# Performance work log

Hardware: AMD Instinct MI355X
Metric: run time of the kernel (lower is better)

Reference implementation:

```python
import jax, jax.numpy as jnp
import numpy as np

N = 50000      # nodes
E = 800000     # edges
IN = 128       # in_channels
H = 64         # hidden (= edge_dim)
OUT = 64       # out_channels
BN_EPS = 1e-5


def _bn(h, gamma, beta):
    # BatchNorm1d in training mode: per-feature batch statistics
    mu = h.mean(axis=0)
    var = h.var(axis=0)
    return gamma * (h - mu) * jax.lax.rsqrt(var + BN_EPS) + beta


def _gine_layer(x, src, dst, edge_attr, We, be, W1, b1, g, bb, W2, b2):
    # edge_attr projected to node feature dim: [E, d_in]
    ea = edge_attr @ We.T + be
    # message: relu(x_j + lin(edge_attr)); x_j = x[src]
    m = jax.nn.relu(x[src] + ea)
    # scatter-add aggregate at destination nodes
    agg = jax.ops.segment_sum(m, dst, num_segments=x.shape[0])
    # (1 + eps) * x_r with eps = 0
    out = agg + x
    # MLP: Linear -> BN -> ReLU -> Linear
    h = jax.nn.relu(_bn(out @ W1.T + b1, g, bb))
    return h @ W2.T + b2


def setup_inputs() -> dict:
    key = jax.random.key(0)
    ks = jax.random.split(key, 12)

    def glorot(k, shape):
        return jax.random.normal(k, shape, jnp.float32) / np.float32(np.sqrt(shape[1]))

    return {
        "x": jax.random.normal(ks[0], (N, IN), jnp.float32),
        "edge_index": jax.random.randint(ks[1], (2, E), 0, N, jnp.int64),
        "edge_attr": jax.random.normal(ks[2], (E, H), jnp.float32),
        # layer 0
        "We0": glorot(ks[3], (IN, H)), "be0": jnp.zeros((IN,), jnp.float32),
        "W1_0": glorot(ks[4], (H, IN)), "b1_0": jnp.zeros((H,), jnp.float32),
        "g0": jnp.ones((H,), jnp.float32), "bb0": jnp.zeros((H,), jnp.float32),
        "W2_0": glorot(ks[5], (H, H)), "b2_0": jnp.zeros((H,), jnp.float32),
        # layer 1
        "We1": glorot(ks[6], (H, H)), "be1": jnp.zeros((H,), jnp.float32),
        "W1_1": glorot(ks[7], (H, H)), "b1_1": jnp.zeros((H,), jnp.float32),
        "g1": jnp.ones((H,), jnp.float32), "bb1": jnp.zeros((H,), jnp.float32),
        "W2_1": glorot(ks[8], (OUT, H)), "b2_1": jnp.zeros((OUT,), jnp.float32),
    }


def reference(x, edge_index, edge_attr,
              We0, be0, W1_0, b1_0, g0, bb0, W2_0, b2_0,
              We1, be1, W1_1, b1_1, g1, bb1, W2_1, b2_1):
    src, dst = edge_index[0], edge_index[1]
    h = _gine_layer(x, src, dst, edge_attr, We0, be0, W1_0, b1_0, g0, bb0, W2_0, b2_0)
    h = jax.nn.relu(h)  # dropout p=0.0 -> identity
    return _gine_layer(h, src, dst, edge_attr, We1, be1, W1_1, b1_1, g1, bb1, W2_1, b2_1)
```

## Files before the change

kernel.cpp:

```cpp
#include <hip/hip_runtime.h>
#include <hip/hip_bf16.h>


typedef short bhalf4 __attribute__((ext_vector_type(4)));
typedef short short8 __attribute__((ext_vector_type(8)));
typedef float f32x4 __attribute__((ext_vector_type(4)));
typedef float f32x2 __attribute__((ext_vector_type(2)));

__device__ __forceinline__ short f2bf(float x) {
    unsigned u = __float_as_uint(x);
    unsigned r = (u + 0x7fffu + ((u >> 16) & 1u)) >> 16;
    return (short)r;
}
__device__ __forceinline__ float bf2f(unsigned short u) {
    return __uint_as_float(((unsigned)u) << 16);
}

__global__ __launch_bounds__(256) void hist_kernel(
    const int* __restrict__ ei, int* __restrict__ cnt, int E)
{
    int e = blockIdx.x * 256 + threadIdx.x;
    if (e < E) atomicAdd(&cnt[ei[E + e]], 1);
}

__global__ __launch_bounds__(1024) void scan_kernel(
    const int* __restrict__ cnt, int* __restrict__ offs,
    int* __restrict__ cursor, int N)
{
    __shared__ int wsum[16];
    __shared__ int chunk_base;
    int tid = threadIdx.x;
    int lane = tid & 63, wid = tid >> 6;
    if (tid == 0) chunk_base = 0;
    __syncthreads();
    for (int start = 0; start < N; start += 1024) {
        int i = start + tid;
        int v = (i < N) ? cnt[i] : 0;
        int s = v;
#pragma unroll
        for (int d = 1; d < 64; d <<= 1) {
            int t = __shfl_up(s, d);
            if (lane >= d) s += t;
        }
        if (lane == 63) wsum[wid] = s;
        __syncthreads();
        int wbase = 0;
        for (int w = 0; w < wid; ++w) wbase += wsum[w];
        int excl = chunk_base + wbase + s - v;
        if (i < N) { offs[i] = excl; cursor[i] = excl; }
        int tot = 0;
        for (int w = 0; w < 16; ++w) tot += wsum[w];
        __syncthreads();
        if (tid == 0) chunk_base += tot;
        __syncthreads();
    }
    if (threadIdx.x == 0) offs[N] = chunk_base;
}

__global__ __launch_bounds__(256) void scatter_kernel(
    const int* __restrict__ ei, int* __restrict__ cursor,
    int* __restrict__ inv, int E)
{
    int e = blockIdx.x * 256 + threadIdx.x;
    if (e >= E) return;
    int d = ei[E + e];
    int pos = atomicAdd(&cursor[d], 1);
    inv[e] = pos;
}

__global__ __launch_bounds__(256) void xcast_kernel(
    const float* __restrict__ x, unsigned short* __restrict__ xb, int total)
{
    for (int i = blockIdx.x * 256 + threadIdx.x; i < total; i += gridDim.x * 256)
        xb[i] = (unsigned short)f2bf(x[i]);
}

template<int DF>
__global__ __launch_bounds__(256) void edgem_kernel(
    const unsigned short* __restrict__ xb,
    const int*    __restrict__ ei,
    const float*  __restrict__ eattr,
    const short*  __restrict__ WB,
    const float*  __restrict__ be,
    const int*    __restrict__ inv,
    unsigned short* __restrict__ pbuf,
    int E)
{
    constexpr int FC  = DF / 16;
    constexpr int LPR = DF / 8;
    constexpr int RPI = 64 / LPR;
    constexpr int NI  = 16 / RPI;
    __shared__ short cm[4][16][DF];
    const int wave = threadIdx.x >> 6;
    const int lane = threadIdx.x & 63;
    const int ebase = (blockIdx.x * 4 + wave) * 16;
    if (ebase >= E) return;
    const int g = lane >> 4, c = lane & 15;
    short* ct = &cm[wave][0][0];
    auto sw = [](int s, int r) { return s ^ ((r >> 1) & 7); };

    int spos[NI], rr[NI], qq[NI];
    short8 xrv[NI];
#pragma unroll
    for (int i = 0; i < NI; ++i) {
        int r = i * RPI + lane / LPR;
        int q = lane % LPR;
        rr[i] = r; qq[i] = q;
        int e = ebase + r;
        bool v = e < E;
        int es = v ? e : (E - 1);
        spos[i] = v ? inv[es] : -1;
        int se = ei[es];
        xrv[i] = *(const short8*)(xb + (size_t)se * DF + q * 8);
    }

    {
        int r = lane >> 2, q = lane & 3;
        int e = ebase + r;
        const float* src = eattr + (size_t)((e < E) ? e : (E - 1)) * 64;
#pragma unroll
        for (int i = 0; i < 4; ++i) {
            f32x4 v = *(const f32x4*)(src + i * 16 + q * 4);
            bhalf4 b;
            b[0] = f2bf(v[0]); b[1] = f2bf(v[1]); b[2] = f2bf(v[2]); b[3] = f2bf(v[3]);
            int s = i * 2 + (q >> 1), h = q & 1;
            *(bhalf4*)(ct + r * DF + sw(s, r) * 8 + h * 4) = b;
        }
    }
    asm volatile("s_waitcnt lgkmcnt(0)" ::: "memory");
    __builtin_amdgcn_sched_barrier(0);

    short8 bfr0 = *(const short8*)(ct + c * DF + sw(g, c) * 8);
    short8 bfr1 = *(const short8*)(ct + c * DF + sw(g + 4, c) * 8);

    f32x4 acc[FC];
#pragma unroll
    for (int fc = 0; fc < FC; ++fc) {
        const short* aw = WB + (size_t)(fc * 16 + c) * 64 + g * 8;
        short8 aw0 = *(const short8*)(aw);
        short8 aw1 = *(const short8*)(aw + 32);
        f32x4 a = {0.f, 0.f, 0.f, 0.f};
        a = __builtin_amdgcn_mfma_f32_16x16x32_bf16(aw0, bfr0, a, 0, 0, 0);
        a = __builtin_amdgcn_mfma_f32_16x16x32_bf16(aw1, bfr1, a, 0, 0, 0);
        acc[fc] = a;
    }

#pragma unroll
    for (int fc = 0; fc < FC; ++fc) {
        f32x4 bev = *(const f32x4*)(be + fc * 16 + g * 4);
        bhalf4 mo;
#pragma unroll
        for (int r = 0; r < 4; ++r)
            mo[r] = f2bf(acc[fc][r] + bev[r]);
        int s = fc * 2 + (g >> 1), h = g & 1;
        *(bhalf4*)(ct + c * DF + sw(s, c) * 8 + h * 4) = mo;
    }
    asm volatile("s_waitcnt lgkmcnt(0)" ::: "memory");
    __builtin_amdgcn_sched_barrier(0);

#pragma unroll
    for (int i = 0; i < NI; ++i) {
        int r = rr[i], q = qq[i];
        short8 v = *(const short8*)(ct + r * DF + sw(q, r) * 8);
        short8 o;
#pragma unroll
        for (int j = 0; j < 8; ++j) {
            float f = bf2f((unsigned short)v[j]) + bf2f((unsigned short)xrv[i][j]);
            o[j] = f2bf(fmaxf(f, 0.f));
        }
        if (spos[i] >= 0)
            *(short8*)(pbuf + (size_t)spos[i] * DF + q * 8) = o;
    }
}

__global__ __launch_bounds__(256) void gathersum0_kernel(
    const unsigned short* __restrict__ pbuf,
    const int* __restrict__ offs,
    const float* __restrict__ x,
    unsigned short* __restrict__ sb, int N)
{
    int wid = threadIdx.x >> 6, lane = threadIdx.x & 63;
    int n = blockIdx.x * 4 + wid;
    if (n >= N) return;
    f32x2 xx = *(const f32x2*)(x + (size_t)n * 128 + 2 * lane);
    float s0 = xx[0], s1 = xx[1];
    int i0 = offs[n], i1 = offs[n + 1];
    const unsigned int* p = (const unsigned int*)(pbuf + (size_t)i0 * 128) + lane;
    int cnt = i1 - i0;
    int i = 0;
    for (; i + 3 < cnt; i += 4) {
        unsigned int v0 = p[0], v1 = p[64], v2 = p[128], v3 = p[192];
        s0 += bf2f((unsigned short)v0) + bf2f((unsigned short)v1)
            + bf2f((unsigned short)v2) + bf2f((unsigned short)v3);
        s1 += bf2f((unsigned short)(v0 >> 16)) + bf2f((unsigned short)(v1 >> 16))
            + bf2f((unsigned short)(v2 >> 16)) + bf2f((unsigned short)(v3 >> 16));
        p += 256;
    }
    for (; i < cnt; ++i) {
        unsigned int v = p[0];
        s0 += bf2f((unsigned short)v);
        s1 += bf2f((unsigned short)(v >> 16));
        p += 64;
    }
    unsigned int packed = (unsigned int)(unsigned short)f2bf(s0)
                        | ((unsigned int)(unsigned short)f2bf(s1) << 16);
    *(unsigned int*)(sb + (size_t)n * 128 + 2 * lane) = packed;
}

__global__ __launch_bounds__(256) void gathersum1_kernel(
    const unsigned short* __restrict__ pbuf,
    const int* __restrict__ offs,
    const float* __restrict__ y0, unsigned short* __restrict__ sb, int N)
{
    int wid = threadIdx.x >> 6, lane = threadIdx.x & 63;
    int n = blockIdx.x * 4 + wid;
    if (n >= N) return;
    float s = y0[(size_t)n * 64 + lane];
    int i0 = offs[n], i1 = offs[n + 1];
    const unsigned short* p = pbuf + (size_t)i0 * 64 + lane;
    int cnt = i1 - i0;
    int i = 0;
    for (; i + 3 < cnt; i += 4) {
        s += bf2f(p[0]) + bf2f(p[64]) + bf2f(p[128]) + bf2f(p[192]);
        p += 256;
    }
    for (; i < cnt; ++i) { s += bf2f(p[0]); p += 64; }
    sb[(size_t)n * 64 + lane] = (unsigned short)f2bf(s);
}

template<int DIN>
__global__ __launch_bounds__(256) void ngemm_kernel(
    const unsigned short* __restrict__ A,
    const short* __restrict__ W, const float* __restrict__ b,
    float* __restrict__ out, int N)
{
    constexpr int KK = DIN / 32;
    const int wave = threadIdx.x >> 6;
    const int lane = threadIdx.x & 63;
    const int nbase = (blockIdx.x * 4 + wave) * 16;
    if (nbase >= N) return;
    const int g = lane >> 4, c = lane & 15;

    int rowc = nbase + c; if (rowc >= N) rowc = N - 1;
    const unsigned short* arow = A + (size_t)rowc * DIN + g * 8;
    short8 afr[KK];
#pragma unroll
    for (int kk = 0; kk < KK; ++kk)
        afr[kk] = *(const short8*)(arow + kk * 32);

#pragma unroll
    for (int cc = 0; cc < 4; ++cc) {
        const float bev = b[cc * 16 + c];
        f32x4 acc = {bev, bev, bev, bev};
#pragma unroll
        for (int kk = 0; kk < KK; ++kk) {
            short8 bw = *(const short8*)(W + (size_t)(cc * 16 + c) * DIN + kk * 32 + g * 8);
            acc = __builtin_amdgcn_mfma_f32_16x16x32_bf16(afr[kk], bw, acc, 0, 0, 0);
        }
#pragma unroll
        for (int r = 0; r < 4; ++r) {
            int row = nbase + g * 4 + r;
            if (row < N) out[(size_t)row * 64 + cc * 16 + c] = acc[r];
        }
    }
}

__global__ __launch_bounds__(256) void ngemm_bn_kernel(
    const float* __restrict__ t, const float* __restrict__ scsh,
    const short* __restrict__ W2, const float* __restrict__ b2,
    float* __restrict__ out, unsigned short* __restrict__ outb,
    int N, int relu_out)
{
    const int wave = threadIdx.x >> 6;
    const int lane = threadIdx.x & 63;
    const int nbase = (blockIdx.x * 4 + wave) * 16;
    if (nbase >= N) return;
    const int g = lane >> 4, c = lane & 15;

    int rowc = nbase + c; if (rowc >= N) rowc = N - 1;
    const float* trow = t + (size_t)rowc * 64 + g * 8;

    short8 afr[2];
#pragma unroll
    for (int kk = 0; kk < 2; ++kk) {
        f32x4 q0 = *(const f32x4*)(trow + kk * 32);
        f32x4 q1 = *(const f32x4*)(trow + kk * 32 + 4);
        const int kbase = kk * 32 + g * 8;
        f32x4 sc0 = *(const f32x4*)(scsh + kbase);
        f32x4 sc1 = *(const f32x4*)(scsh + kbase + 4);
        f32x4 sh0 = *(const f32x4*)(scsh + 64 + kbase);
        f32x4 sh1 = *(const f32x4*)(scsh + 64 + kbase + 4);
#pragma unroll
        for (int j = 0; j < 4; ++j) {
            afr[kk][j]     = f2bf(fmaxf(q0[j] * sc0[j] + sh0[j], 0.f));
            afr[kk][j + 4] = f2bf(fmaxf(q1[j] * sc1[j] + sh1[j], 0.f));
        }
    }

#pragma unroll
    for (int cc = 0; cc < 4; ++cc) {
        const float bev = b2[cc * 16 + c];
        f32x4 acc = {bev, bev, bev, bev};
#pragma unroll
        for (int kk = 0; kk < 2; ++kk) {
            short8 bw = *(const short8*)(W2 + (size_t)(cc * 16 + c) * 64 + kk * 32 + g * 8);
            acc = __builtin_amdgcn_mfma_f32_16x16x32_bf16(afr[kk], bw, acc, 0, 0, 0);
        }
#pragma unroll
        for (int r = 0; r < 4; ++r) {
            int row = nbase + g * 4 + r;
            if (row < N) {
                float v = acc[r];
                if (relu_out) {
                    v = fmaxf(v, 0.f);
                    outb[(size_t)row * 64 + cc * 16 + c] = (unsigned short)f2bf(v);
                }
                out[(size_t)row * 64 + cc * 16 + c] = v;
            }
        }
    }
}

__global__ __launch_bounds__(256) void bnstats_kernel(
    const float* __restrict__ t, float* __restrict__ sums, int total)
{
    int tid = threadIdx.x;
    float s = 0.f, s2 = 0.f;
    for (int i = blockIdx.x * 256 + tid; i < total; i += gridDim.x * 256) {
        float v = t[i];
        s += v; s2 += v * v;
    }
    __shared__ float ls[256], ls2[256];
    ls[tid] = s; ls2[tid] = s2;
    __syncthreads();
    if (tid < 64) {
        s  = ls[tid]  + ls[tid + 64]  + ls[tid + 128]  + ls[tid + 192];
        s2 = ls2[tid] + ls2[tid + 64] + ls2[tid + 128] + ls2[tid + 192];
        atomicAdd(&sums[tid], s);
        atomicAdd(&sums[64 + tid], s2);
    }
}

__global__ void bnfinal_kernel(const float* __restrict__ sums,
                               const float* __restrict__ g,
                               const float* __restrict__ bb,
                               float* __restrict__ scsh, float invN)
{
    int f = threadIdx.x;
    float mean = sums[f] * invN;
    float var  = sums[64 + f] * invN - mean * mean;
    float sc = g[f] * rsqrtf(var + 1e-5f);
    scsh[f] = sc;
    scsh[64 + f] = bb[f] - mean * sc;
}

__global__ __launch_bounds__(256) void prep_kernel(
    const float* __restrict__ We0, const float* __restrict__ W1_0,
    const float* __restrict__ We1, const float* __restrict__ W1_1,
    const float* __restrict__ W2_0, const float* __restrict__ W2_1,
    short* __restrict__ WeB0, short* __restrict__ W1B0,
    short* __restrict__ WeB1, short* __restrict__ W1B1,
    short* __restrict__ W2B0, short* __restrict__ W2B1)
{
    int i = blockIdx.x * 256 + threadIdx.x;
    if (i < 128 * 64) WeB0[i] = f2bf(We0[i]);
    if (i < 64 * 128) W1B0[i] = f2bf(W1_0[i]);
    if (i < 64 * 64) {
        WeB1[i] = f2bf(We1[i]);
        W1B1[i] = f2bf(W1_1[i]);
        W2B0[i] = f2bf(W2_0[i]);
        W2B1[i] = f2bf(W2_1[i]);
    }
}

extern "C" void kernel_launch(void* const* d_in, const int* in_sizes, int n_in,
                              void* d_out, int out_size, void* d_ws, size_t ws_size,
                              hipStream_t stream)
{
    (void)n_in; (void)out_size; (void)ws_size;
    const float* x     = (const float*)d_in[0];
    const int*   ei    = (const int*)d_in[1];
    const float* eattr = (const float*)d_in[2];
    const float* We0   = (const float*)d_in[3];
    const float* be0   = (const float*)d_in[4];
    const float* W1_0  = (const float*)d_in[5];
    const float* b1_0  = (const float*)d_in[6];
    const float* g0    = (const float*)d_in[7];
    const float* bb0   = (const float*)d_in[8];
    const float* W2_0  = (const float*)d_in[9];
    const float* b2_0  = (const float*)d_in[10];
    const float* We1   = (const float*)d_in[11];
    const float* be1   = (const float*)d_in[12];
    const float* W1_1  = (const float*)d_in[13];
    const float* b1_1  = (const float*)d_in[14];
    const float* g1    = (const float*)d_in[15];
    const float* bb1   = (const float*)d_in[16];
    const float* W2_1  = (const float*)d_in[17];
    const float* b2_1  = (const float*)d_in[18];
    float* out = (float*)d_out;

    const int N = in_sizes[0] / 128;
    const int E = in_sizes[2] / 64;

    char* ws = (char*)d_ws;
    size_t o = 0;
    auto alloc = [&](size_t bytes) { char* p = ws + o; o = (o + bytes + 255) & ~(size_t)255; return p; };
    unsigned short* pbuf = (unsigned short*)alloc((size_t)E * 128 * 2);
    float* tbuf   = (float*)alloc((size_t)N * 64 * 4);
    float* y0     = (float*)alloc((size_t)N * 64 * 4);
    unsigned short* xb = (unsigned short*)alloc((size_t)N * 128 * 2);
    unsigned short* yb = (unsigned short*)alloc((size_t)N * 64 * 2);
    short* WeB0   = (short*)alloc(128 * 64 * 2);
    short* W1B0   = (short*)alloc(64 * 128 * 2);
    short* WeB1   = (short*)alloc(64 * 64 * 2);
    short* W1B1   = (short*)alloc(64 * 64 * 2);
    short* W2B0   = (short*)alloc(64 * 64 * 2);
    short* W2B1   = (short*)alloc(64 * 64 * 2);
    float* stats  = (float*)alloc(512 * 4);
    int*   cnt    = (int*)alloc((size_t)N * 4);
    int*   offs   = (int*)alloc((size_t)(N + 1) * 4);
    int*   inv    = (int*)alloc((size_t)E * 4);
    float* sum0  = stats;
    float* scsh0 = stats + 128;
    float* sum1  = stats + 256;
    float* scsh1 = stats + 384;
    unsigned short* sb0 = xb;
    unsigned short* sb1 = yb;

    (void)hipMemsetAsync(stats, 0, 512 * 4, stream);
    (void)hipMemsetAsync(cnt, 0, (size_t)N * 4, stream);
    prep_kernel<<<64, 256, 0, stream>>>(We0, W1_0, We1, W1_1, W2_0, W2_1,
                                        WeB0, W1B0, WeB1, W1B1, W2B0, W2B1);
    xcast_kernel<<<2048, 256, 0, stream>>>(x, xb, N * 128);

    const int eb256 = (E + 255) / 256;

    hist_kernel<<<eb256, 256, 0, stream>>>(ei, cnt, E);
    scan_kernel<<<1, 1024, 0, stream>>>(cnt, offs, cnt, N);
    scatter_kernel<<<eb256, 256, 0, stream>>>(ei, cnt, inv, E);

    const int edge_blocks = ((E + 15) / 16 + 3) / 4;
    const int n4_blocks   = (N + 3) / 4;
    const int nt_blocks   = ((N + 15) / 16 + 3) / 4;

    edgem_kernel<128><<<edge_blocks, 256, 0, stream>>>(
        xb, ei, eattr, WeB0, be0, inv, pbuf, E);
    gathersum0_kernel<<<n4_blocks, 256, 0, stream>>>(pbuf, offs, x, sb0, N);
    ngemm_kernel<128><<<nt_blocks, 256, 0, stream>>>(sb0, W1B0, b1_0, tbuf, N);
    bnstats_kernel<<<256, 256, 0, stream>>>(tbuf, sum0, N * 64);
    bnfinal_kernel<<<1, 64, 0, stream>>>(sum0, g0, bb0, scsh0, 1.0f / N);
    ngemm_bn_kernel<<<nt_blocks, 256, 0, stream>>>(
        tbuf, scsh0, W2B0, b2_0, y0, yb, N, 1);

    edgem_kernel<64><<<edge_blocks, 256, 0, stream>>>(
        yb, ei, eattr, WeB1, be1, inv, pbuf, E);
    gathersum1_kernel<<<n4_blocks, 256, 0, stream>>>(pbuf, offs, y0, sb1, N);
    ngemm_kernel<64><<<nt_blocks, 256, 0, stream>>>(sb1, W1B1, b1_1, tbuf, N);
    bnstats_kernel<<<256, 256, 0, stream>>>(tbuf, sum1, N * 64);
    bnfinal_kernel<<<1, 64, 0, stream>>>(sum1, g1, bb1, scsh1, 1.0f / N);
    ngemm_bn_kernel<<<nt_blocks, 256, 0, stream>>>(
        tbuf, scsh1, W2B1, b2_1, out, yb, N, 0);
}
```

Before: 534.5 us.

## Fuse BN statistics into GEMM epilogue and merge prep/cast kernels

The node GEMM now accumulates per-feature sum and sum-of-squares in its epilogue using shuffles and atomics, which removes the separate bnstats pass over tbuf. The BN scale/shift is recomputed inside the second GEMM, which removes the bnfinal launch. Weight conversion and the x cast are merged into one launch. The edge kernel now issues the eattr load and LDS staging before the gathers and uses a changed swizzle. In exchange there are many more global atomics on 128 addresses and redundant per-thread rsqrt work.

```diff
diff --git a/kernel.cpp b/kernel.cpp
--- a/kernel.cpp
+++ b/kernel.cpp
@@ -68,11 +68,26 @@
     inv[e] = pos;
 }
 
-__global__ __launch_bounds__(256) void xcast_kernel(
+__global__ __launch_bounds__(256) void prep_kernel(
+    const float* __restrict__ We0, const float* __restrict__ W1_0,
+    const float* __restrict__ We1, const float* __restrict__ W1_1,
+    const float* __restrict__ W2_0, const float* __restrict__ W2_1,
+    short* __restrict__ WeB0, short* __restrict__ W1B0,
+    short* __restrict__ WeB1, short* __restrict__ W1B1,
+    short* __restrict__ W2B0, short* __restrict__ W2B1,
     const float* __restrict__ x, unsigned short* __restrict__ xb, int total)
 {
-    for (int i = blockIdx.x * 256 + threadIdx.x; i < total; i += gridDim.x * 256)
-        xb[i] = (unsigned short)f2bf(x[i]);
+    int i = blockIdx.x * 256 + threadIdx.x;
+    if (i < 128 * 64) WeB0[i] = f2bf(We0[i]);
+    if (i < 64 * 128) W1B0[i] = f2bf(W1_0[i]);
+    if (i < 64 * 64) {
+        WeB1[i] = f2bf(We1[i]);
+        W1B1[i] = f2bf(W1_1[i]);
+        W2B0[i] = f2bf(W2_0[i]);
+        W2B1[i] = f2bf(W2_1[i]);
+    }
+    for (int k = i; k < total; k += gridDim.x * 256)
+        xb[k] = (unsigned short)f2bf(x[k]);
 }
 
 template<int DF>
@@ -97,7 +112,21 @@
     if (ebase >= E) return;
     const int g = lane >> 4, c = lane & 15;
     short* ct = &cm[wave][0][0];
-    auto sw = [](int s, int r) { return s ^ ((r >> 1) & 7); };
+    auto sw = [](int s, int r) { return s ^ (r & 7); };
+
+    {
+        int r = lane >> 2, q = lane & 3;
+        int e = ebase + r;
+        const float* src = eattr + (size_t)((e < E) ? e : (E - 1)) * 64;
+#pragma unroll
+        for (int i = 0; i < 4; ++i) {
+            f32x4 v = *(const f32x4*)(src + i * 16 + q * 4);
+            bhalf4 b;
+            b[0] = f2bf(v[0]); b[1] = f2bf(v[1]); b[2] = f2bf(v[2]); b[3] = f2bf(v[3]);
+            int s = i * 2 + (q >> 1), h = q & 1;
+            *(bhalf4*)(ct + r * DF + sw(s, r) * 8 + h * 4) = b;
+        }
+    }
 
     int spos[NI], rr[NI], qq[NI];
     short8 xrv[NI];
@@ -112,20 +141,6 @@
         spos[i] = v ? inv[es] : -1;
         int se = ei[es];
         xrv[i] = *(const short8*)(xb + (size_t)se * DF + q * 8);
-    }
-
-    {
-        int r = lane >> 2, q = lane & 3;
-        int e = ebase + r;
-        const float* src = eattr + (size_t)((e < E) ? e : (E - 1)) * 64;
-#pragma unroll
-        for (int i = 0; i < 4; ++i) {
-            f32x4 v = *(const f32x4*)(src + i * 16 + q * 4);
-            bhalf4 b;
-            b[0] = f2bf(v[0]); b[1] = f2bf(v[1]); b[2] = f2bf(v[2]); b[3] = f2bf(v[3]);
-            int s = i * 2 + (q >> 1), h = q & 1;
-            *(bhalf4*)(ct + r * DF + sw(s, r) * 8 + h * 4) = b;
-        }
     }
     asm volatile("s_waitcnt lgkmcnt(0)" ::: "memory");
     __builtin_amdgcn_sched_barrier(0);
@@ -232,7 +247,7 @@
 __global__ __launch_bounds__(256) void ngemm_kernel(
     const unsigned short* __restrict__ A,
     const short* __restrict__ W, const float* __restrict__ b,
-    float* __restrict__ out, int N)
+    float* __restrict__ out, float* __restrict__ sums, int N)
 {
     constexpr int KK = DIN / 32;
     const int wave = threadIdx.x >> 6;
@@ -257,19 +272,31 @@
             short8 bw = *(const short8*)(W + (size_t)(cc * 16 + c) * DIN + kk * 32 + g * 8);
             acc = __builtin_amdgcn_mfma_f32_16x16x32_bf16(afr[kk], bw, acc, 0, 0, 0);
         }
+        float sv = 0.f, qv = 0.f;
 #pragma unroll
         for (int r = 0; r < 4; ++r) {
             int row = nbase + g * 4 + r;
-            if (row < N) out[(size_t)row * 64 + cc * 16 + c] = acc[r];
+            if (row < N) {
+                float v = acc[r];
+                out[(size_t)row * 64 + cc * 16 + c] = v;
+                sv += v; qv += v * v;
+            }
+        }
+        sv += __shfl_xor(sv, 16); sv += __shfl_xor(sv, 32);
+        qv += __shfl_xor(qv, 16); qv += __shfl_xor(qv, 32);
+        if (g == 0) {
+            atomicAdd(&sums[cc * 16 + c], sv);
+            atomicAdd(&sums[64 + cc * 16 + c], qv);
         }
     }
 }
 
 __global__ __launch_bounds__(256) void ngemm_bn_kernel(
-    const float* __restrict__ t, const float* __restrict__ scsh,
+    const float* __restrict__ t, const float* __restrict__ sums,
+    const float* __restrict__ gam, const float* __restrict__ bet,
     const short* __restrict__ W2, const float* __restrict__ b2,
     float* __restrict__ out, unsigned short* __restrict__ outb,
-    int N, int relu_out)
+    int N, int relu_out, float invN)
 {
     const int wave = threadIdx.x >> 6;
     const int lane = threadIdx.x & 63;
@@ -286,14 +313,15 @@
         f32x4 q0 = *(const f32x4*)(trow + kk * 32);
         f32x4 q1 = *(const f32x4*)(trow + kk * 32 + 4);
         const int kbase = kk * 32 + g * 8;
-        f32x4 sc0 = *(const f32x4*)(scsh + kbase);
-        f32x4 sc1 = *(const f32x4*)(scsh + kbase + 4);
-        f32x4 sh0 = *(const f32x4*)(scsh + 64 + kbase);
-        f32x4 sh1 = *(const f32x4*)(scsh + 64 + kbase + 4);
-#pragma unroll
-        for (int j = 0; j < 4; ++j) {
-            afr[kk][j]     = f2bf(fmaxf(q0[j] * sc0[j] + sh0[j], 0.f));
-            afr[kk][j + 4] = f2bf(fmaxf(q1[j] * sc1[j] + sh1[j], 0.f));
+#pragma unroll
+        for (int j = 0; j < 8; ++j) {
+            int f = kbase + j;
+            float mean = sums[f] * invN;
+            float var  = sums[64 + f] * invN - mean * mean;
+            float sc = gam[f] * rsqrtf(var + 1e-5f);
+            float sh = bet[f] - mean * sc;
+            float q = (j < 4) ? q0[j] : q1[j - 4];
+            afr[kk][j] = f2bf(fmaxf(q * sc + sh, 0.f));
         }
     }
 
@@ -318,58 +346,6 @@
                 out[(size_t)row * 64 + cc * 16 + c] = v;
             }
         }
-    }
-}
-
-__global__ __launch_bounds__(256) void bnstats_kernel(
-    const float* __restrict__ t, float* __restrict__ sums, int total)
-{
-    int tid = threadIdx.x;
-    float s = 0.f, s2 = 0.f;
-    for (int i = blockIdx.x * 256 + tid; i < total; i += gridDim.x * 256) {
-        float v = t[i];
-        s += v; s2 += v * v;
-    }
-    __shared__ float ls[256], ls2[256];
-    ls[tid] = s; ls2[tid] = s2;
-    __syncthreads();
-    if (tid < 64) {
-        s  = ls[tid]  + ls[tid + 64]  + ls[tid + 128]  + ls[tid + 192];
-        s2 = ls2[tid] + ls2[tid + 64] + ls2[tid + 128] + ls2[tid + 192];
-        atomicAdd(&sums[tid], s);
-        atomicAdd(&sums[64 + tid], s2);
-    }
-}
-
-__global__ void bnfinal_kernel(const float* __restrict__ sums,
-                               const float* __restrict__ g,
-                               const float* __restrict__ bb,
-                               float* __restrict__ scsh, float invN)
-{
-    int f = threadIdx.x;
-    float mean = sums[f] * invN;
-    float var  = sums[64 + f] * invN - mean * mean;
-    float sc = g[f] * rsqrtf(var + 1e-5f);
-    scsh[f] = sc;
-    scsh[64 + f] = bb[f] - mean * sc;
-}
-
-__global__ __launch_bounds__(256) void prep_kernel(
-    const float* __restrict__ We0, const float* __restrict__ W1_0,
-    const float* __restrict__ We1, const float* __restrict__ W1_1,
-    const float* __restrict__ W2_0, const float* __restrict__ W2_1,
-    short* __restrict__ WeB0, short* __restrict__ W1B0,
-    short* __restrict__ WeB1, short* __restrict__ W1B1,
-    short* __restrict__ W2B0, short* __restrict__ W2B1)
-{
-    int i = blockIdx.x * 256 + threadIdx.x;
-    if (i < 128 * 64) WeB0[i] = f2bf(We0[i]);
-    if (i < 64 * 128) W1B0[i] = f2bf(W1_0[i]);
-    if (i < 64 * 64) {
-        WeB1[i] = f2bf(We1[i]);
-        W1B1[i] = f2bf(W1_1[i]);
-        W2B0[i] = f2bf(W2_0[i]);
-        W2B1[i] = f2bf(W2_1[i]);
     }
 }
 
@@ -421,17 +397,15 @@
     int*   offs   = (int*)alloc((size_t)(N + 1) * 4);
     int*   inv    = (int*)alloc((size_t)E * 4);
     float* sum0  = stats;
-    float* scsh0 = stats + 128;
-    float* sum1  = stats + 256;
-    float* scsh1 = stats + 384;
+    float* sum1  = stats + 128;
     unsigned short* sb0 = xb;
     unsigned short* sb1 = yb;
 
     (void)hipMemsetAsync(stats, 0, 512 * 4, stream);
     (void)hipMemsetAsync(cnt, 0, (size_t)N * 4, stream);
-    prep_kernel<<<64, 256, 0, stream>>>(We0, W1_0, We1, W1_1, W2_0, W2_1,
-                                        WeB0, W1B0, WeB1, W1B1, W2B0, W2B1);
-    xcast_kernel<<<2048, 256, 0, stream>>>(x, xb, N * 128);
+    prep_kernel<<<2048, 256, 0, stream>>>(We0, W1_0, We1, W1_1, W2_0, W2_1,
+                                          WeB0, W1B0, WeB1, W1B1, W2B0, W2B1,
+                                          x, xb, N * 128);
 
     const int eb256 = (E + 255) / 256;
 
@@ -446,18 +420,14 @@
     edgem_kernel<128><<<edge_blocks, 256, 0, stream>>>(
         xb, ei, eattr, WeB0, be0, inv, pbuf, E);
     gathersum0_kernel<<<n4_blocks, 256, 0, stream>>>(pbuf, offs, x, sb0, N);
-    ngemm_kernel<128><<<nt_blocks, 256, 0, stream>>>(sb0, W1B0, b1_0, tbuf, N);
-    bnstats_kernel<<<256, 256, 0, stream>>>(tbuf, sum0, N * 64);
-    bnfinal_kernel<<<1, 64, 0, stream>>>(sum0, g0, bb0, scsh0, 1.0f / N);
+    ngemm_kernel<128><<<nt_blocks, 256, 0, stream>>>(sb0, W1B0, b1_0, tbuf, sum0, N);
     ngemm_bn_kernel<<<nt_blocks, 256, 0, stream>>>(
-        tbuf, scsh0, W2B0, b2_0, y0, yb, N, 1);
+        tbuf, sum0, g0, bb0, W2B0, b2_0, y0, yb, N, 1, 1.0f / N);
 
     edgem_kernel<64><<<edge_blocks, 256, 0, stream>>>(
         yb, ei, eattr, WeB1, be1, inv, pbuf, E);
     gathersum1_kernel<<<n4_blocks, 256, 0, stream>>>(pbuf, offs, y0, sb1, N);
-    ngemm_kernel<64><<<nt_blocks, 256, 0, stream>>>(sb1, W1B1, b1_1, tbuf, N);
-    bnstats_kernel<<<256, 256, 0, stream>>>(tbuf, sum1, N * 64);
-    bnfinal_kernel<<<1, 64, 0, stream>>>(sum1, g1, bb1, scsh1, 1.0f / N);
+    ngemm_kernel<64><<<nt_blocks, 256, 0, stream>>>(sb1, W1B1, b1_1, tbuf, sum1, N);
     ngemm_bn_kernel<<<nt_blocks, 256, 0, stream>>>(
-        tbuf, scsh1, W2B1, b2_1, out, yb, N, 0);
-}
+        tbuf, sum1, g1, bb1, W2B1, b2_1, out, yb, N, 0, 1.0f / N);
+}
```

Result: slower. 674.0 us (+26.1%).

## Push layer-0 W1 projection onto edges before aggregation to halve message width

Applied to the files above, without the earlier changes.

Uses linearity to apply W1 to each layer-0 message inside the edge kernel, so messages are stored and aggregated at 64 features instead of 128. The node-side term x@W1+b1 is computed by a separate GEMM and added during the gather. This cuts pbuf write and gather traffic in half, at the cost of an extra per-edge MFMA GEMM and one more bf16 rounding before summation. It also folds the x cast into the weight-prep kernel and changes the LDS swizzle.

```diff
diff --git a/kernel.cpp b/kernel.cpp
--- a/kernel.cpp
+++ b/kernel.cpp
@@ -68,11 +68,144 @@
     inv[e] = pos;
 }
 
-__global__ __launch_bounds__(256) void xcast_kernel(
+__global__ __launch_bounds__(256) void prep_kernel(
+    const float* __restrict__ We0, const float* __restrict__ W1_0,
+    const float* __restrict__ We1, const float* __restrict__ W1_1,
+    const float* __restrict__ W2_0, const float* __restrict__ W2_1,
+    short* __restrict__ WeB0, short* __restrict__ W1B0,
+    short* __restrict__ WeB1, short* __restrict__ W1B1,
+    short* __restrict__ W2B0, short* __restrict__ W2B1,
     const float* __restrict__ x, unsigned short* __restrict__ xb, int total)
 {
-    for (int i = blockIdx.x * 256 + threadIdx.x; i < total; i += gridDim.x * 256)
-        xb[i] = (unsigned short)f2bf(x[i]);
+    int i = blockIdx.x * 256 + threadIdx.x;
+    if (i < 128 * 64) WeB0[i] = f2bf(We0[i]);
+    if (i < 64 * 128) W1B0[i] = f2bf(W1_0[i]);
+    if (i < 64 * 64) {
+        WeB1[i] = f2bf(We1[i]);
+        W1B1[i] = f2bf(W1_1[i]);
+        W2B0[i] = f2bf(W2_0[i]);
+        W2B1[i] = f2bf(W2_1[i]);
+    }
+    for (int k = i; k < total; k += gridDim.x * 256)
+        xb[k] = (unsigned short)f2bf(x[k]);
+}
+
+__global__ __launch_bounds__(256) void edgem0_kernel(
+    const unsigned short* __restrict__ xb,
+    const int*    __restrict__ ei,
+    const float*  __restrict__ eattr,
+    const short*  __restrict__ WeB,
+    const float*  __restrict__ be,
+    const short*  __restrict__ W1B,
+    const int*    __restrict__ inv,
+    unsigned short* __restrict__ pbuf,
+    int E)
+{
+    __shared__ short at_s[4][16][64];
+    __shared__ short xm_s[4][16][128];
+    const int wave = threadIdx.x >> 6;
+    const int lane = threadIdx.x & 63;
+    const int ebase = (blockIdx.x * 4 + wave) * 16;
+    if (ebase >= E) return;
+    const int g = lane >> 4, c = lane & 15;
+    short* at = &at_s[wave][0][0];
+    short* xm = &xm_s[wave][0][0];
+    auto sw = [](int s, int r) { return s ^ (r & 7); };
+
+    int spos[2];
+#pragma unroll
+    for (int i = 0; i < 2; ++i) {
+        int r = i * 8 + (lane >> 3);
+        int e = ebase + r;
+        spos[i] = (e < E) ? inv[e] : -1;
+    }
+
+    {
+        int r = lane >> 2, q = lane & 3;
+        int e = ebase + r;
+        const float* src = eattr + (size_t)((e < E) ? e : (E - 1)) * 64;
+#pragma unroll
+        for (int i = 0; i < 4; ++i) {
+            f32x4 v = *(const f32x4*)(src + i * 16 + q * 4);
+            bhalf4 b;
+            b[0] = f2bf(v[0]); b[1] = f2bf(v[1]); b[2] = f2bf(v[2]); b[3] = f2bf(v[3]);
+            int s = i * 2 + (q >> 1), h = q & 1;
+            *(bhalf4*)(at + r * 64 + sw(s, r) * 8 + h * 4) = b;
+        }
+    }
+
+#pragma unroll
+    for (int i = 0; i < 4; ++i) {
+        int r = i * 4 + (lane >> 4);
+        int q = lane & 15;
+        int e = ebase + r;
+        int es = (e < E) ? e : (E - 1);
+        int se = ei[es];
+        short8 v = *(const short8*)(xb + (size_t)se * 128 + q * 8);
+        *(short8*)(xm + r * 128 + sw(q, r) * 8) = v;
+    }
+    asm volatile("s_waitcnt lgkmcnt(0)" ::: "memory");
+    __builtin_amdgcn_sched_barrier(0);
+
+    short8 bfr0 = *(const short8*)(at + c * 64 + sw(g, c) * 8);
+    short8 bfr1 = *(const short8*)(at + c * 64 + sw(g + 4, c) * 8);
+
+    f32x4 acc[8];
+#pragma unroll
+    for (int fc = 0; fc < 8; ++fc) {
+        const short* aw = WeB + (size_t)(fc * 16 + c) * 64 + g * 8;
+        short8 aw0 = *(const short8*)(aw);
+        short8 aw1 = *(const short8*)(aw + 32);
+        f32x4 a = {0.f, 0.f, 0.f, 0.f};
+        a = __builtin_amdgcn_mfma_f32_16x16x32_bf16(aw0, bfr0, a, 0, 0, 0);
+        a = __builtin_amdgcn_mfma_f32_16x16x32_bf16(aw1, bfr1, a, 0, 0, 0);
+        acc[fc] = a;
+    }
+
+#pragma unroll
+    for (int fc = 0; fc < 8; ++fc) {
+        f32x4 bev = *(const f32x4*)(be + fc * 16 + g * 4);
+        int s = fc * 2 + (g >> 1);
+        short* addr = xm + c * 128 + sw(s, c) * 8 + (g & 1) * 4;
+        bhalf4 xv = *(const bhalf4*)(addr);
+        bhalf4 mo;
+#pragma unroll
+        for (int r = 0; r < 4; ++r)
+            mo[r] = f2bf(fmaxf(acc[fc][r] + bev[r] + bf2f((unsigned short)xv[r]), 0.f));
+        *(bhalf4*)(addr) = mo;
+    }
+    asm volatile("s_waitcnt lgkmcnt(0)" ::: "memory");
+    __builtin_amdgcn_sched_barrier(0);
+
+    short8 b2[4];
+#pragma unroll
+    for (int kk = 0; kk < 4; ++kk)
+        b2[kk] = *(const short8*)(xm + c * 128 + sw(kk * 4 + g, c) * 8);
+
+#pragma unroll
+    for (int fc2 = 0; fc2 < 4; ++fc2) {
+        f32x4 a = {0.f, 0.f, 0.f, 0.f};
+#pragma unroll
+        for (int kk = 0; kk < 4; ++kk) {
+            short8 aw = *(const short8*)(W1B + (size_t)(fc2 * 16 + c) * 128 + kk * 32 + g * 8);
+            a = __builtin_amdgcn_mfma_f32_16x16x32_bf16(aw, b2[kk], a, 0, 0, 0);
+        }
+        bhalf4 po;
+#pragma unroll
+        for (int r = 0; r < 4; ++r) po[r] = f2bf(a[r]);
+        *(bhalf4*)(at + c * 64 + sw(fc2 * 2 + (g >> 1), c) * 8 + (g & 1) * 4) = po;
+    }
+    asm volatile("s_waitcnt lgkmcnt(0)" ::: "memory");
+    __builtin_amdgcn_sched_barrier(0);
+
+#pragma unroll
+    for (int i = 0; i < 2; ++i) {
+        int r = i * 8 + (lane >> 3);
+        int q = lane & 7;
+        short8 v = *(const short8*)(at + r * 64 + sw(q, r) * 8);
+        if (spos[i] >= 0)
+            *(short8*)(pbuf + (size_t)spos[i] * 64 + q * 8) = v;
+    }
 }
 
 template<int DF>
@@ -97,7 +230,21 @@
     if (ebase >= E) return;
     const int g = lane >> 4, c = lane & 15;
     short* ct = &cm[wave][0][0];
-    auto sw = [](int s, int r) { return s ^ ((r >> 1) & 7); };
+    auto sw = [](int s, int r) { return s ^ (r & 7); };
+
+    {
+        int r = lane >> 2, q = lane & 3;
+        int e = ebase + r;
+        const float* src = eattr + (size_t)((e < E) ? e : (E - 1)) * 64;
+#pragma unroll
+        for (int i = 0; i < 4; ++i) {
+            f32x4 v = *(const f32x4*)(src + i * 16 + q * 4);
+            bhalf4 b;
+            b[0] = f2bf(v[0]); b[1] = f2bf(v[1]); b[2] = f2bf(v[2]); b[3] = f2bf(v[3]);
+            int s = i * 2 + (q >> 1), h = q & 1;
+            *(bhalf4*)(ct + r * DF + sw(s, r) * 8 + h * 4) = b;
+        }
+    }
 
     int spos[NI], rr[NI], qq[NI];
     short8 xrv[NI];
@@ -113,20 +260,6 @@
         int se = ei[es];
         xrv[i] = *(const short8*)(xb + (size_t)se * DF + q * 8);
     }
-
-    {
-        int r = lane >> 2, q = lane & 3;
-        int e = ebase + r;
-        const float* src = eattr + (size_t)((e < E) ? e : (E - 1)) * 64;
-#pragma unroll
-        for (int i = 0; i < 4; ++i) {
-            f32x4 v = *(const f32x4*)(src + i * 16 + q * 4);
-            bhalf4 b;
-            b[0] = f2bf(v[0]); b[1] = f2bf(v[1]); b[2] = f2bf(v[2]); b[3] = f2bf(v[3]);
-            int s = i * 2 + (q >> 1), h = q & 1;
-            *(bhalf4*)(ct + r * DF + sw(s, r) * 8 + h * 4) = b;
-        }
-    }
     asm volatile("s_waitcnt lgkmcnt(0)" ::: "memory");
     __builtin_amdgcn_sched_barrier(0);
 
@@ -173,38 +306,25 @@
     }
 }
 
-__global__ __launch_bounds__(256) void gathersum0_kernel(
+__global__ __launch_bounds__(256) void gather0_kernel(
     const unsigned short* __restrict__ pbuf,
     const int* __restrict__ offs,
-    const float* __restrict__ x,
-    unsigned short* __restrict__ sb, int N)
+    const float* __restrict__ xw1, float* __restrict__ t, int N)
 {
     int wid = threadIdx.x >> 6, lane = threadIdx.x & 63;
     int n = blockIdx.x * 4 + wid;
     if (n >= N) return;
-    f32x2 xx = *(const f32x2*)(x + (size_t)n * 128 + 2 * lane);
-    float s0 = xx[0], s1 = xx[1];
+    float acc = xw1[(size_t)n * 64 + lane];
     int i0 = offs[n], i1 = offs[n + 1];
-    const unsigned int* p = (const unsigned int*)(pbuf + (size_t)i0 * 128) + lane;
+    const unsigned short* p = pbuf + (size_t)i0 * 64 + lane;
     int cnt = i1 - i0;
     int i = 0;
     for (; i + 3 < cnt; i += 4) {
-        unsigned int v0 = p[0], v1 = p[64], v2 = p[128], v3 = p[192];
-        s0 += bf2f((unsigned short)v0) + bf2f((unsigned short)v1)
-            + bf2f((unsigned short)v2) + bf2f((unsigned short)v3);
-        s1 += bf2f((unsigned short)(v0 >> 16)) + bf2f((unsigned short)(v1 >> 16))
-            + bf2f((unsigned short)(v2 >> 16)) + bf2f((unsigned short)(v3 >> 16));
+        acc += bf2f(p[0]) + bf2f(p[64]) + bf2f(p[128]) + bf2f(p[192]);
         p += 256;
     }
-    for (; i < cnt; ++i) {
-        unsigned int v = p[0];
-        s0 += bf2f((unsigned short)v);
-        s1 += bf2f((unsigned short)(v >> 16));
-        p += 64;
-    }
-    unsigned int packed = (unsigned int)(unsigned short)f2bf(s0)
-                        | ((unsigned int)(unsigned short)f2bf(s1) << 16);
-    *(unsigned int*)(sb + (size_t)n * 128 + 2 * lane) = packed;
+    for (; i < cnt; ++i) { acc += bf2f(p[0]); p += 64; }
+    t[(size_t)n * 64 + lane] = acc;
 }
 
 __global__ __launch_bounds__(256) void gathersum1_kernel(
@@ -352,25 +472,6 @@
     float sc = g[f] * rsqrtf(var + 1e-5f);
     scsh[f] = sc;
     scsh[64 + f] = bb[f] - mean * sc;
-}
-
-__global__ __launch_bounds__(256) void prep_kernel(
-    const float* __restrict__ We0, const float* __restrict__ W1_0,
-    const float* __restrict__ We1, const float* __restrict__ W1_1,
-    const float* __restrict__ W2_0, const float* __restrict__ W2_1,
-    short* __restrict__ WeB0, short* __restrict__ W1B0,
-    short* __restrict__ WeB1, short* __restrict__ W1B1,
-    short* __restrict__ W2B0, short* __restrict__ W2B1)
-{
-    int i = blockIdx.x * 256 + threadIdx.x;
-    if (i < 128 * 64) WeB0[i] = f2bf(We0[i]);
-    if (i < 64 * 128) W1B0[i] = f2bf(W1_0[i]);
-    if (i < 64 * 64) {
-        WeB1[i] = f2bf(We1[i]);
-        W1B1[i] = f2bf(W1_1[i]);
-        W2B0[i] = f2bf(W2_0[i]);
-        W2B1[i] = f2bf(W2_1[i]);
-    }
 }
 
 extern "C" void kernel_launch(void* const* d_in, const int* in_sizes, int n_in,
@@ -405,7 +506,7 @@
     char* ws = (char*)d_ws;
     size_t o = 0;
     auto alloc = [&](size_t bytes) { char* p = ws + o; o = (o + bytes + 255) & ~(size_t)255; return p; };
-    unsigned short* pbuf = (unsigned short*)alloc((size_t)E * 128 * 2);
+    unsigned short* pbuf = (unsigned short*)alloc((size_t)E * 64 * 2);
     float* tbuf   = (float*)alloc((size_t)N * 64 * 4);
     float* y0     = (float*)alloc((size_t)N * 64 * 4);
     unsigned short* xb = (unsigned short*)alloc((size_t)N * 128 * 2);
@@ -424,14 +525,14 @@
     float* scsh0 = stats + 128;
     float* sum1  = stats + 256;
     float* scsh1 = stats + 384;
-    unsigned short* sb0 = xb;
+    float* xw1f  = y0;
     unsigned short* sb1 = yb;
 
     (void)hipMemsetAsync(stats, 0, 512 * 4, stream);
     (void)hipMemsetAsync(cnt, 0, (size_t)N * 4, stream);
-    prep_kernel<<<64, 256, 0, stream>>>(We0, W1_0, We1, W1_1, W2_0, W2_1,
-                                        WeB0, W1B0, WeB1, W1B1, W2B0, W2B1);
-    xcast_kernel<<<2048, 256, 0, stream>>>(x, xb, N * 128);
+    prep_kernel<<<2048, 256, 0, stream>>>(We0, W1_0, We1, W1_1, W2_0, W2_1,
+                                          WeB0, W1B0, WeB1, W1B1, W2B0, W2B1,
+                                          x, xb, N * 128);
 
     const int eb256 = (E + 255) / 256;
 
@@ -443,10 +544,10 @@
     const int n4_blocks   = (N + 3) / 4;
     const int nt_blocks   = ((N + 15) / 16 + 3) / 4;
 
-    edgem_kernel<128><<<edge_blocks, 256, 0, stream>>>(
-        xb, ei, eattr, WeB0, be0, inv, pbuf, E);
-    gathersum0_kernel<<<n4_blocks, 256, 0, stream>>>(pbuf, offs, x, sb0, N);
-    ngemm_kernel<128><<<nt_blocks, 256, 0, stream>>>(sb0, W1B0, b1_0, tbuf, N);
+    edgem0_kernel<<<edge_blocks, 256, 0, stream>>>(
+        xb, ei, eattr, WeB0, be0, W1B0, inv, pbuf, E);
+    ngemm_kernel<128><<<nt_blocks, 256, 0, stream>>>(xb, W1B0, b1_0, xw1f, N);
+    gather0_kernel<<<n4_blocks, 256, 0, stream>>>(pbuf, offs, xw1f, tbuf, N);
     bnstats_kernel<<<256, 256, 0, stream>>>(tbuf, sum0, N * 64);
     bnfinal_kernel<<<1, 64, 0, stream>>>(sum0, g0, bb0, scsh0, 1.0f / N);
     ngemm_bn_kernel<<<nt_blocks, 256, 0, stream>>>(
```

Result: slower. 603.5 us (+12.9%).

## Process two edge tiles per wave in edge kernel and fuse weight prep with x cast

Applied to the files above, without the earlier changes.

Each wave in the edge-message kernel now handles 32 edges (two 16-edge tiles) rather than 16. The weight fragments are loaded once and reused across both tiles, and more gather loads can be in flight at the same time. The weight bf16 conversion is merged into the x-cast kernel, which removes one launch, and the LDS swizzle pattern changes to r&7. The cost is doubled LDS per wave and higher register pressure, which may lower occupancy.

```diff
diff --git a/kernel.cpp b/kernel.cpp
--- a/kernel.cpp
+++ b/kernel.cpp
@@ -68,15 +68,30 @@
     inv[e] = pos;
 }
 
-__global__ __launch_bounds__(256) void xcast_kernel(
+__global__ __launch_bounds__(256) void prep_kernel(
+    const float* __restrict__ We0, const float* __restrict__ W1_0,
+    const float* __restrict__ We1, const float* __restrict__ W1_1,
+    const float* __restrict__ W2_0, const float* __restrict__ W2_1,
+    short* __restrict__ WeB0, short* __restrict__ W1B0,
+    short* __restrict__ WeB1, short* __restrict__ W1B1,
+    short* __restrict__ W2B0, short* __restrict__ W2B1,
     const float* __restrict__ x, unsigned short* __restrict__ xb, int total)
 {
-    for (int i = blockIdx.x * 256 + threadIdx.x; i < total; i += gridDim.x * 256)
-        xb[i] = (unsigned short)f2bf(x[i]);
+    int i = blockIdx.x * 256 + threadIdx.x;
+    if (i < 128 * 64) WeB0[i] = f2bf(We0[i]);
+    if (i < 64 * 128) W1B0[i] = f2bf(W1_0[i]);
+    if (i < 64 * 64) {
+        WeB1[i] = f2bf(We1[i]);
+        W1B1[i] = f2bf(W1_1[i]);
+        W2B0[i] = f2bf(W2_0[i]);
+        W2B1[i] = f2bf(W2_1[i]);
+    }
+    for (int k = i; k < total; k += gridDim.x * 256)
+        xb[k] = (unsigned short)f2bf(x[k]);
 }
 
 template<int DF>
-__global__ __launch_bounds__(256) void edgem_kernel(
+__global__ __launch_bounds__(256) void edgem2_kernel(
     const unsigned short* __restrict__ xb,
     const int*    __restrict__ ei,
     const float*  __restrict__ eattr,
@@ -90,86 +105,105 @@
     constexpr int LPR = DF / 8;
     constexpr int RPI = 64 / LPR;
     constexpr int NI  = 16 / RPI;
-    __shared__ short cm[4][16][DF];
+    __shared__ short cm[4][2][16][DF];
     const int wave = threadIdx.x >> 6;
     const int lane = threadIdx.x & 63;
-    const int ebase = (blockIdx.x * 4 + wave) * 16;
-    if (ebase >= E) return;
+    const int tbase = (blockIdx.x * 4 + wave) * 32;
+    if (tbase >= E) return;
     const int g = lane >> 4, c = lane & 15;
-    short* ct = &cm[wave][0][0];
-    auto sw = [](int s, int r) { return s ^ ((r >> 1) & 7); };
-
-    int spos[NI], rr[NI], qq[NI];
-    short8 xrv[NI];
-#pragma unroll
-    for (int i = 0; i < NI; ++i) {
-        int r = i * RPI + lane / LPR;
-        int q = lane % LPR;
-        rr[i] = r; qq[i] = q;
-        int e = ebase + r;
-        bool v = e < E;
-        int es = v ? e : (E - 1);
-        spos[i] = v ? inv[es] : -1;
-        int se = ei[es];
-        xrv[i] = *(const short8*)(xb + (size_t)se * DF + q * 8);
-    }
+    short* ct0 = &cm[wave][0][0][0];
+    short* ct1 = &cm[wave][1][0][0];
+    auto sw = [](int s, int r) { return s ^ (r & 7); };
 
     {
         int r = lane >> 2, q = lane & 3;
-        int e = ebase + r;
-        const float* src = eattr + (size_t)((e < E) ? e : (E - 1)) * 64;
-#pragma unroll
-        for (int i = 0; i < 4; ++i) {
-            f32x4 v = *(const f32x4*)(src + i * 16 + q * 4);
-            bhalf4 b;
-            b[0] = f2bf(v[0]); b[1] = f2bf(v[1]); b[2] = f2bf(v[2]); b[3] = f2bf(v[3]);
-            int s = i * 2 + (q >> 1), h = q & 1;
-            *(bhalf4*)(ct + r * DF + sw(s, r) * 8 + h * 4) = b;
+#pragma unroll
+        for (int t = 0; t < 2; ++t) {
+            short* ct = t ? ct1 : ct0;
+            int e = tbase + t * 16 + r;
+            const float* src = eattr + (size_t)((e < E) ? e : (E - 1)) * 64;
+#pragma unroll
+            for (int i = 0; i < 4; ++i) {
+                f32x4 v = *(const f32x4*)(src + i * 16 + q * 4);
+                bhalf4 b;
+                b[0] = f2bf(v[0]); b[1] = f2bf(v[1]); b[2] = f2bf(v[2]); b[3] = f2bf(v[3]);
+                int s = i * 2 + (q >> 1), h = q & 1;
+                *(bhalf4*)(ct + r * DF + sw(s, r) * 8 + h * 4) = b;
+            }
+        }
+    }
+
+    short8 xrv[2][NI];
+    int spos[2][NI];
+    const int r0 = lane / LPR, qx = lane % LPR;
+#pragma unroll
+    for (int t = 0; t < 2; ++t) {
+#pragma unroll
+        for (int i = 0; i < NI; ++i) {
+            int r = i * RPI + r0;
+            int e = tbase + t * 16 + r;
+            bool v = e < E;
+            int es = v ? e : (E - 1);
+            spos[t][i] = v ? inv[es] : -1;
+            int se = ei[es];
+            xrv[t][i] = *(const short8*)(xb + (size_t)se * DF + qx * 8);
         }
     }
     asm volatile("s_waitcnt lgkmcnt(0)" ::: "memory");
     __builtin_amdgcn_sched_barrier(0);
 
-    short8 bfr0 = *(const short8*)(ct + c * DF + sw(g, c) * 8);
-    short8 bfr1 = *(const short8*)(ct + c * DF + sw(g + 4, c) * 8);
-
-    f32x4 acc[FC];
+    short8 b00 = *(const short8*)(ct0 + c * DF + sw(g, c) * 8);
+    short8 b01 = *(const short8*)(ct0 + c * DF + sw(g + 4, c) * 8);
+    short8 b10 = *(const short8*)(ct1 + c * DF + sw(g, c) * 8);
+    short8 b11 = *(const short8*)(ct1 + c * DF + sw(g + 4, c) * 8);
+
+    f32x4 acc0[FC], acc1[FC];
 #pragma unroll
     for (int fc = 0; fc < FC; ++fc) {
         const short* aw = WB + (size_t)(fc * 16 + c) * 64 + g * 8;
         short8 aw0 = *(const short8*)(aw);
         short8 aw1 = *(const short8*)(aw + 32);
-        f32x4 a = {0.f, 0.f, 0.f, 0.f};
-        a = __builtin_amdgcn_mfma_f32_16x16x32_bf16(aw0, bfr0, a, 0, 0, 0);
-        a = __builtin_amdgcn_mfma_f32_16x16x32_bf16(aw1, bfr1, a, 0, 0, 0);
-        acc[fc] = a;
+        f32x4 a0 = {0.f, 0.f, 0.f, 0.f};
+        f32x4 a1 = {0.f, 0.f, 0.f, 0.f};
+        a0 = __builtin_amdgcn_mfma_f32_16x16x32_bf16(aw0, b00, a0, 0, 0, 0);
+        a1 = __builtin_amdgcn_mfma_f32_16x16x32_bf16(aw0, b10, a1, 0, 0, 0);
+        a0 = __builtin_amdgcn_mfma_f32_16x16x32_bf16(aw1, b01, a0, 0, 0, 0);
+        a1 = __builtin_amdgcn_mfma_f32_16x16x32_bf16(aw1, b11, a1, 0, 0, 0);
+        acc0[fc] = a0; acc1[fc] = a1;
     }
 
 #pragma unroll
     for (int fc = 0; fc < FC; ++fc) {
         f32x4 bev = *(const f32x4*)(be + fc * 16 + g * 4);
-        bhalf4 mo;
-#pragma unroll
-        for (int r = 0; r < 4; ++r)
-            mo[r] = f2bf(acc[fc][r] + bev[r]);
+        bhalf4 m0, m1;
+#pragma unroll
+        for (int r = 0; r < 4; ++r) {
+            m0[r] = f2bf(acc0[fc][r] + bev[r]);
+            m1[r] = f2bf(acc1[fc][r] + bev[r]);
+        }
         int s = fc * 2 + (g >> 1), h = g & 1;
-        *(bhalf4*)(ct + c * DF + sw(s, c) * 8 + h * 4) = mo;
+        *(bhalf4*)(ct0 + c * DF + sw(s, c) * 8 + h * 4) = m0;
+        *(bhalf4*)(ct1 + c * DF + sw(s, c) * 8 + h * 4) = m1;
     }
     asm volatile("s_waitcnt lgkmcnt(0)" ::: "memory");
     __builtin_amdgcn_sched_barrier(0);
 
 #pragma unroll
-    for (int i = 0; i < NI; ++i) {
-        int r = rr[i], q = qq[i];
-        short8 v = *(const short8*)(ct + r * DF + sw(q, r) * 8);
-        short8 o;
-#pragma unroll
-        for (int j = 0; j < 8; ++j) {
-            float f = bf2f((unsigned short)v[j]) + bf2f((unsigned short)xrv[i][j]);
-            o[j] = f2bf(fmaxf(f, 0.f));
-        }
-        if (spos[i] >= 0)
-            *(short8*)(pbuf + (size_t)spos[i] * DF + q * 8) = o;
+    for (int t = 0; t < 2; ++t) {
+        short* ct = t ? ct1 : ct0;
+#pragma unroll
+        for (int i = 0; i < NI; ++i) {
+            int r = i * RPI + r0;
+            short8 v = *(const short8*)(ct + r * DF + sw(qx, r) * 8);
+            short8 o;
+#pragma unroll
+            for (int j = 0; j < 8; ++j) {
+                float f = bf2f((unsigned short)v[j]) + bf2f((unsigned short)xrv[t][i][j]);
+                o[j] = f2bf(fmaxf(f, 0.f));
+            }
+            if (spos[t][i] >= 0)
+                *(short8*)(pbuf + (size_t)spos[t][i] * DF + qx * 8) = o;
+        }
     }
 }
 
@@ -352,25 +386,6 @@
     float sc = g[f] * rsqrtf(var + 1e-5f);
     scsh[f] = sc;
     scsh[64 + f] = bb[f] - mean * sc;
-}
-
-__global__ __launch_bounds__(256) void prep_kernel(
-    const float* __restrict__ We0, const float* __restrict__ W1_0,
-    const float* __restrict__ We1, const float* __restrict__ W1_1,
-    const float* __restrict__ W2_0, const float* __restrict__ W2_1,
-    short* __restrict__ WeB0, short* __restrict__ W1B0,
-    short* __restrict__ WeB1, short* __restrict__ W1B1,
-    short* __restrict__ W2B0, short* __restrict__ W2B1)
-{
-    int i = blockIdx.x * 256 + threadIdx.x;
-    if (i < 128 * 64) WeB0[i] = f2bf(We0[i]);
-    if (i < 64 * 128) W1B0[i] = f2bf(W1_0[i]);
-    if (i < 64 * 64) {
-        WeB1[i] = f2bf(We1[i]);
-        W1B1[i] = f2bf(W1_1[i]);
-        W2B0[i] = f2bf(W2_0[i]);
-        W2B1[i] = f2bf(W2_1[i]);
-    }
 }
 
 extern "C" void kernel_launch(void* const* d_in, const int* in_sizes, int n_in,
@@ -429,9 +444,9 @@
 
     (void)hipMemsetAsync(stats, 0, 512 * 4, stream);
     (void)hipMemsetAsync(cnt, 0, (size_t)N * 4, stream);
-    prep_kernel<<<64, 256, 0, stream>>>(We0, W1_0, We1, W1_1, W2_0, W2_1,
-                                        WeB0, W1B0, WeB1, W1B1, W2B0, W2B1);
-    xcast_kernel<<<2048, 256, 0, stream>>>(x, xb, N * 128);
+    prep_kernel<<<2048, 256, 0, stream>>>(We0, W1_0, We1, W1_1, W2_0, W2_1,
+                                          WeB0, W1B0, WeB1, W1B1, W2B0, W2B1,
+                                          x, xb, N * 128);
 
     const int eb256 = (E + 255) / 256;
 
@@ -439,11 +454,11 @@
     scan_kernel<<<1, 1024, 0, stream>>>(cnt, offs, cnt, N);
     scatter_kernel<<<eb256, 256, 0, stream>>>(ei, cnt, inv, E);
 
-    const int edge_blocks = ((E + 15) / 16 + 3) / 4;
+    const int edge_blocks = (((E + 31) / 32) + 3) / 4;
     const int n4_blocks   = (N + 3) / 4;
     const int nt_blocks   = ((N + 15) / 16 + 3) / 4;
 
-    edgem_kernel<128><<<edge_blocks, 256, 0, stream>>>(
+    edgem2_kernel<128><<<edge_blocks, 256, 0, stream>>>(
         xb, ei, eattr, WeB0, be0, inv, pbuf, E);
     gathersum0_kernel<<<n4_blocks, 256, 0, stream>>>(pbuf, offs, x, sb0, N);
     ngemm_kernel<128><<<nt_blocks, 256, 0, stream>>>(sb0, W1B0, b1_0, tbuf, N);
@@ -452,7 +467,7 @@
     ngemm_bn_kernel<<<nt_blocks, 256, 0, stream>>>(
         tbuf, scsh0, W2B0, b2_0, y0, yb, N, 1);
 
-    edgem_kernel<64><<<edge_blocks, 256, 0, stream>>>(
+    edgem2_kernel<64><<<edge_blocks, 256, 0, stream>>>(
         yb, ei, eattr, WeB1, be1, inv, pbuf, E);
     gathersum1_kernel<<<n4_blocks, 256, 0, stream>>>(pbuf, offs, y0, sb1, N);
     ngemm_kernel<64><<<nt_blocks, 256, 0, stream>>>(sb1, W1B1, b1_1, tbuf, N);
```

After: 555.6 us. 4.0% more time.
